# Optimization experiments

Hardware: AMD Instinct MI355X
Metric: run time of the kernel (lower is better)

Reference implementation:

```python
import jax, jax.numpy as jnp
import numpy as np
from jax import lax

BLANK = 0
LOGZERO = -1e30  # finite stand-in for -inf (keeps grads NaN-free, exact in fp32 logaddexp)


def setup_inputs() -> dict:
    key = jax.random.key(0)
    k1, k2 = jax.random.split(key)
    T, B, V, S = 512, 32, 4096, 128
    logits = jax.random.normal(k1, (T, B, V), dtype=jnp.float32)
    log_probs = jax.nn.log_softmax(logits, axis=-1)
    targets = jax.random.randint(k2, (B, S), 1, V, dtype=jnp.int32)  # avoid blank label
    input_lengths = jnp.full((B,), T, dtype=jnp.int32)   # must be >= 2*S+1
    target_lengths = jnp.full((B,), S, dtype=jnp.int32)
    return {"log_probs": log_probs, "targets": targets,
            "input_lengths": input_lengths, "target_lengths": target_lengths}


def _shift_right(a, n):
    # a: (B, L) log-space; shift states right by n, filling with log(0)
    pad = jnp.full(a.shape[:-1] + (n,), LOGZERO, dtype=a.dtype)
    return jnp.concatenate([pad, a[..., :-n]], axis=-1)


def _ctc_log_likelihood(log_probs, targets, input_lengths, target_lengths):
    # Vectorized CTC forward (alpha) recursion over the blank-interleaved trellis.
    # Mathematically identical to the per-sample bounded DP in the torch module:
    # states outside the reachability bounds carry log(0) / never feed the terminal sum.
    T, B, V = log_probs.shape
    S = targets.shape[1]
    L = 2 * S + 1
    blanked = jnp.full((B, L), BLANK, dtype=jnp.int32).at[:, 1::2].set(targets)
    # emission log-prob of each trellis state at each time: (T, B, L)
    emit = jnp.take_along_axis(log_probs, jnp.broadcast_to(blanked[None], (T, B, L)), axis=2)
    idx = jnp.arange(L)
    # skip transition (j-2 -> j) allowed for label states whose label differs from previous label
    skip = (idx % 2 == 1) & (idx >= 2) & (blanked != jnp.roll(blanked, 2, axis=1))  # (B, L)

    alpha0 = jnp.full((B, L), LOGZERO, dtype=log_probs.dtype)
    alpha0 = alpha0.at[:, 0].set(emit[0, :, 0]).at[:, 1].set(emit[0, :, 1])

    def step(alpha, xs):
        emit_t, t = xs  # emit_t: (B, L)
        pre = jnp.logaddexp(alpha, _shift_right(alpha, 1))
        pre = jnp.where(skip, jnp.logaddexp(pre, _shift_right(alpha, 2)), pre)
        new = emit_t + pre
        new = jnp.where((t < input_lengths)[:, None], new, alpha)  # freeze past each sample's length
        return new, None

    alpha, _ = lax.scan(step, alpha0, (emit[1:], jnp.arange(1, T)))
    b = jnp.arange(B)
    end = 2 * target_lengths  # final blank state index per sample
    ll = jnp.logaddexp(alpha[b, end], alpha[b, end - 1])  # log p(target | input)
    return ll


def reference(log_probs, targets, input_lengths, target_lengths):
    ll = _ctc_log_likelihood(log_probs, targets, input_lengths, target_lengths)
    B = log_probs.shape[1]
    # faithful to the module's 'mean' branch: (ret / target_lengths / B).sum()  (NOT negated)
    return (ll / target_lengths.astype(ll.dtype) / B).sum()
```

## Files before the change

kernel.cpp:

```cpp
#include <hip/hip_runtime.h>
#include <hip/hip_bf16.h>
#include <cstdint>

typedef unsigned short u16;
typedef uint32_t u32;

constexpr int Tc = 512, Bc = 32, Vc = 4096, Sc = 128;
constexpr int BOOST = 13;
constexpr int DPF = 16;
constexpr float LOG2E = 1.4426950408889634f;
constexpr float LN2 = 0.6931471805599453f;

__device__ __forceinline__ float bfs(u32 s) { return __uint_as_float(s << 16); }
__device__ __forceinline__ float bflo(u32 p) { return __uint_as_float(p << 16); }
__device__ __forceinline__ float bfhi(u32 p) { return __uint_as_float(p & 0xffff0000u); }

__device__ __forceinline__ u16 f2bf(float f) {
    __hip_bfloat16 h = __float2bfloat16(f);
    return *reinterpret_cast<u16*>(&h);
}

__global__ __launch_bounds__(128) void k_gather(const float* __restrict__ lp,
                                                const int* __restrict__ tgt,
                                                u16* __restrict__ emitT,
                                                u16* __restrict__ blankT) {
    const int t = blockIdx.x;
    const int b = blockIdx.y;
    const float* row = lp + ((size_t)t * Bc + b) * Vc;
    const int s = threadIdx.x;
    const int lab = tgt[b * Sc + s];
    const float e = __builtin_amdgcn_exp2f(fmaf(row[lab], LOG2E, (float)BOOST));
    emitT[((size_t)b * Tc + t) * Sc + s] = f2bf(e);
    if (s == 0) {
        const float eb = __builtin_amdgcn_exp2f(fmaf(row[0], LOG2E, (float)BOOST));
        blankT[(size_t)b * Tc + t] = f2bf(eb);
    }
}

template <int CTRL, int RMASK>
__device__ __forceinline__ float dppmax(float v) {
    int t = __builtin_amdgcn_update_dpp(__float_as_int(v), __float_as_int(v),
                                        CTRL, RMASK, 0xf, false);
    return fmaxf(v, __int_as_float(t));
}
__device__ __forceinline__ float wave_max_bcast(float v) {
    v = dppmax<0x111, 0xf>(v);
    v = dppmax<0x112, 0xf>(v);
    v = dppmax<0x114, 0xf>(v);
    v = dppmax<0x118, 0xf>(v);
    v = dppmax<0x142, 0xa>(v);
    v = dppmax<0x143, 0xc>(v);
    return __int_as_float(__builtin_amdgcn_readlane(__float_as_int(v), 63));
}

__global__ __launch_bounds__(64) void k_ctc(const u16* __restrict__ emitT,
                                            const u16* __restrict__ blankT,
                                            const int* __restrict__ tgt,
                                            const int* __restrict__ in_len,
                                            const int* __restrict__ tg_len,
                                            float* __restrict__ out) {
    const int b = blockIdx.x;
    const int lane = threadIdx.x;
    const u32* prow = reinterpret_cast<const u32*>(emitT + (size_t)b * Tc * Sc);
    const u16* brow = blankT + (size_t)b * Tc;

    const int tg0 = tgt[b * Sc + 2 * lane];
    const int tg1 = tgt[b * Sc + 2 * lane + 1];
    const int tgm = (lane > 0) ? tgt[b * Sc + 2 * lane - 1] : tg0;
    const float m1 = (lane > 0 && tg0 != tgm) ? 1.f : 0.f;
    const float m3 = (tg1 != tg0) ? 1.f : 0.f;
    const float sel = (lane == 63) ? 1.f : 0.f;

    const int steps = min(in_len[b], Tc) - 1;

    const u32 p0 = prow[lane];
    float a0 = (lane == 0) ? bfs(brow[0]) : 0.f;
    float a1 = (lane == 0) ? bflo(p0) : 0.f;
    float a2 = 0.f, a3 = 0.f, a4 = 0.f;
    int e_acc = 0;

    u32 pk[DPF];
    u32 bk[DPF];
#pragma unroll
    for (int d = 0; d < DPF; ++d) {
        int tt = 1 + d;
        if (tt > steps) tt = (steps > 0) ? steps : 0;
        pk[d] = prow[(size_t)tt * 64 + lane];
        bk[d] = brow[tt];
    }

#define STEP(d) {                                                   \
        const float e1 = bflo(pk[d]);                               \
        const float e3 = bfhi(pk[d]);                               \
        const float ebl = bfs(bk[d]);                               \
        int tn = t + DPF; if (tn > steps) tn = steps;               \
        pk[d] = prow[(size_t)tn * 64 + lane];                       \
        bk[d] = brow[tn];                                           \
        float sh = __shfl_up(a3, 1);                                \
        if (lane == 0) sh = 0.f;                                    \
        const float s01 = a0 + a1;                                  \
        const float s12 = a1 + a2;                                  \
        const float s23 = a2 + a3;                                  \
        const float n0 = ebl * (a0 + sh);                           \
        const float n1 = e1 * fmaf(m1, sh, s01);                    \
        const float n2 = ebl * s12;                                 \
        const float n3 = e3 * fmaf(m3, a1, s23);                    \
        const float n4 = ebl * fmaf(sel, a3, a4);                   \
        const bool live = (t <= steps);                             \
        a0 = live ? n0 : a0; a1 = live ? n1 : a1;                   \
        a2 = live ? n2 : a2; a3 = live ? n3 : a3;                   \
        a4 = live ? n4 : a4;                                        \
        ++t; }

#define RENORM() {                                                  \
        float m = fmaxf(fmaxf(fmaxf(a0, a1), fmaxf(a2, a3)), a4);   \
        m = wave_max_bcast(m);                                      \
        int e = (int)((__float_as_uint(m) >> 23) & 0xffu) - 127;    \
        float scale = __uint_as_float((u32)(127 - e) << 23);        \
        a0 *= scale; a1 *= scale; a2 *= scale;                      \
        a3 *= scale; a4 *= scale;                                   \
        e_acc += e; }

    int t = 1;
    const int ngroups = (steps + 7) / 8;
    const int npair = (ngroups + 1) / 2;
    for (int gp = 0; gp < npair; ++gp) {
#pragma unroll
        for (int d = 0; d < 8; ++d) STEP(d)
        RENORM()
#pragma unroll
        for (int d = 8; d < 16; ++d) STEP(d)
        RENORM()
    }
#undef STEP
#undef RENORM

    __shared__ float sa[257];
    sa[4 * lane + 0] = a0;
    sa[4 * lane + 1] = a1;
    sa[4 * lane + 2] = a2;
    sa[4 * lane + 3] = a3;
    if (lane == 63) sa[256] = a4;
    __syncthreads();
    if (lane == 0) {
        const int tl = tg_len[b];
        const int ei = 2 * tl;
        const float ssum = sa[ei] + sa[ei - 1];
        const float ll = __logf(ssum) +
                         LN2 * ((float)e_acc - (float)BOOST * (float)(steps + 1));
        atomicAdd(out, ll / (float)tl / (float)Bc);
    }
}

extern "C" void kernel_launch(void* const* d_in, const int* in_sizes, int n_in,
                              void* d_out, int out_size, void* d_ws, size_t ws_size,
                              hipStream_t stream) {
    const float* lp = (const float*)d_in[0];
    const int* tgt = (const int*)d_in[1];
    const int* in_len = (const int*)d_in[2];
    const int* tg_len = (const int*)d_in[3];

    char* ws = (char*)d_ws;
    u16* blankT = (u16*)ws;
    u16* emitT = (u16*)(ws + 64 * 1024);

    (void)hipMemsetAsync(d_out, 0, sizeof(float), stream);
    k_gather<<<dim3(Tc, Bc), 128, 0, stream>>>(lp, tgt, emitT, blankT);
    k_ctc<<<Bc, 64, 0, stream>>>(emitT, blankT, tgt, in_len, tg_len, (float*)d_out);
}
```

Measured before the change: 384.2 us.

## Stage log-prob rows in LDS, keep blank emissions in fp32, streamline the CTC step loop

The gather kernel now copies each full vocabulary row into shared memory with coalesced float4 loads, then gathers label emissions from LDS. Before, each thread gathered directly from global memory at random label offsets. Blank emissions are stored and read as fp32 instead of bf16. In the recurrence, the lane shift moves from __shfl_up to a DPP row-shift that fills lane 0 with zero. The steady-state loop drops the per-step liveness selects and index clamps, with a separate guarded tail block handling the last 16 steps. The trade-off: the gather reads the whole 256 MB tensor densely, and the unclamped prefetch reads one time step past the last valid one.

```diff
diff --git a/kernel.cpp b/kernel.cpp
--- a/kernel.cpp
+++ b/kernel.cpp
@@ -11,7 +11,6 @@
 constexpr float LOG2E = 1.4426950408889634f;
 constexpr float LN2 = 0.6931471805599453f;
 
-__device__ __forceinline__ float bfs(u32 s) { return __uint_as_float(s << 16); }
 __device__ __forceinline__ float bflo(u32 p) { return __uint_as_float(p << 16); }
 __device__ __forceinline__ float bfhi(u32 p) { return __uint_as_float(p & 0xffff0000u); }
 
@@ -20,20 +19,28 @@
     return *reinterpret_cast<u16*>(&h);
 }
 
-__global__ __launch_bounds__(128) void k_gather(const float* __restrict__ lp,
+__global__ __launch_bounds__(256) void k_gather(const float* __restrict__ lp,
                                                 const int* __restrict__ tgt,
                                                 u16* __restrict__ emitT,
-                                                u16* __restrict__ blankT) {
+                                                float* __restrict__ blankT) {
+    __shared__ float row[Vc];
     const int t = blockIdx.x;
     const int b = blockIdx.y;
-    const float* row = lp + ((size_t)t * Bc + b) * Vc;
+    const float4* src4 = reinterpret_cast<const float4*>(lp + ((size_t)t * Bc + b) * Vc);
+    float4* row4 = reinterpret_cast<float4*>(row);
+#pragma unroll
+    for (int i = 0; i < Vc / 4 / 256; ++i)
+        row4[threadIdx.x + i * 256] = src4[threadIdx.x + i * 256];
+    __syncthreads();
     const int s = threadIdx.x;
-    const int lab = tgt[b * Sc + s];
-    const float e = __builtin_amdgcn_exp2f(fmaf(row[lab], LOG2E, (float)BOOST));
-    emitT[((size_t)b * Tc + t) * Sc + s] = f2bf(e);
+    if (s < Sc) {
+        const int lab = tgt[b * Sc + s];
+        const float e = __builtin_amdgcn_exp2f(fmaf(row[lab], LOG2E, (float)BOOST));
+        emitT[((size_t)b * Tc + t) * Sc + s] = f2bf(e);
+    }
     if (s == 0) {
-        const float eb = __builtin_amdgcn_exp2f(fmaf(row[0], LOG2E, (float)BOOST));
-        blankT[(size_t)b * Tc + t] = f2bf(eb);
+        blankT[(size_t)b * Tc + t] =
+            __builtin_amdgcn_exp2f(fmaf(row[0], LOG2E, (float)BOOST));
     }
 }
 
@@ -53,8 +60,13 @@
     return __int_as_float(__builtin_amdgcn_readlane(__float_as_int(v), 63));
 }
 
+__device__ __forceinline__ float wave_shr1(float v) {
+    return __int_as_float(__builtin_amdgcn_update_dpp(
+        0, __float_as_int(v), 0x138, 0xf, 0xf, true));
+}
+
 __global__ __launch_bounds__(64) void k_ctc(const u16* __restrict__ emitT,
-                                            const u16* __restrict__ blankT,
+                                            const float* __restrict__ blankT,
                                             const int* __restrict__ tgt,
                                             const int* __restrict__ in_len,
                                             const int* __restrict__ tg_len,
@@ -62,7 +74,7 @@
     const int b = blockIdx.x;
     const int lane = threadIdx.x;
     const u32* prow = reinterpret_cast<const u32*>(emitT + (size_t)b * Tc * Sc);
-    const u16* brow = blankT + (size_t)b * Tc;
+    const float* brow = blankT + (size_t)b * Tc;
 
     const int tg0 = tgt[b * Sc + 2 * lane];
     const int tg1 = tgt[b * Sc + 2 * lane + 1];
@@ -74,30 +86,41 @@
     const int steps = min(in_len[b], Tc) - 1;
 
     const u32 p0 = prow[lane];
-    float a0 = (lane == 0) ? bfs(brow[0]) : 0.f;
+    float a0 = (lane == 0) ? brow[0] : 0.f;
     float a1 = (lane == 0) ? bflo(p0) : 0.f;
     float a2 = 0.f, a3 = 0.f, a4 = 0.f;
     int e_acc = 0;
 
     u32 pk[DPF];
-    u32 bk[DPF];
+    float bk[DPF];
 #pragma unroll
     for (int d = 0; d < DPF; ++d) {
-        int tt = 1 + d;
-        if (tt > steps) tt = (steps > 0) ? steps : 0;
-        pk[d] = prow[(size_t)tt * 64 + lane];
-        bk[d] = brow[tt];
+        pk[d] = prow[(size_t)(1 + d) * 64 + lane];
+        bk[d] = brow[1 + d];
     }
 
-#define STEP(d) {                                                   \
+#define STEP_N(d) {                                                 \
         const float e1 = bflo(pk[d]);                               \
         const float e3 = bfhi(pk[d]);                               \
-        const float ebl = bfs(bk[d]);                               \
-        int tn = t + DPF; if (tn > steps) tn = steps;               \
-        pk[d] = prow[(size_t)tn * 64 + lane];                       \
-        bk[d] = brow[tn];                                           \
-        float sh = __shfl_up(a3, 1);                                \
-        if (lane == 0) sh = 0.f;                                    \
+        const float ebl = bk[d];                                    \
+        pk[d] = prow[(size_t)(t + DPF) * 64 + lane];                \
+        bk[d] = brow[t + DPF];                                      \
+        const float sh = wave_shr1(a3);                             \
+        const float s01 = a0 + a1;                                  \
+        const float s12 = a1 + a2;                                  \
+        const float s23 = a2 + a3;                                  \
+        const float n0 = ebl * (a0 + sh);                           \
+        const float n1 = e1 * fmaf(m1, sh, s01);                    \
+        const float n3 = e3 * fmaf(m3, a1, s23);                    \
+        a4 = ebl * fmaf(sel, a3, a4);                               \
+        a0 = n0; a1 = n1; a2 = ebl * s12; a3 = n3;                  \
+        ++t; }
+
+#define STEP_T(d) {                                                 \
+        const float e1 = bflo(pk[d]);                               \
+        const float e3 = bfhi(pk[d]);                               \
+        const float ebl = bk[d];                                    \
+        const float sh = wave_shr1(a3);                             \
         const float s01 = a0 + a1;                                  \
         const float s12 = a1 + a2;                                  \
         const float s23 = a2 + a3;                                  \
@@ -122,17 +145,23 @@
         e_acc += e; }
 
     int t = 1;
-    const int ngroups = (steps + 7) / 8;
-    const int npair = (ngroups + 1) / 2;
-    for (int gp = 0; gp < npair; ++gp) {
+    const int nfull = steps >> 4;
+    for (int g = 0; g < nfull; ++g) {
 #pragma unroll
-        for (int d = 0; d < 8; ++d) STEP(d)
+        for (int d = 0; d < 8; ++d) STEP_N(d)
         RENORM()
 #pragma unroll
-        for (int d = 8; d < 16; ++d) STEP(d)
+        for (int d = 8; d < 16; ++d) STEP_N(d)
         RENORM()
     }
-#undef STEP
+#pragma unroll
+    for (int d = 0; d < 8; ++d) STEP_T(d)
+    RENORM()
+#pragma unroll
+    for (int d = 8; d < 16; ++d) STEP_T(d)
+    RENORM()
+#undef STEP_N
+#undef STEP_T
 #undef RENORM
 
     __shared__ float sa[257];
@@ -161,10 +190,10 @@
     const int* tg_len = (const int*)d_in[3];
 
     char* ws = (char*)d_ws;
-    u16* blankT = (u16*)ws;
-    u16* emitT = (u16*)(ws + 64 * 1024);
+    float* blankT = (float*)ws;
+    u16* emitT = (u16*)(ws + 128 * 1024);
 
     (void)hipMemsetAsync(d_out, 0, sizeof(float), stream);
-    k_gather<<<dim3(Tc, Bc), 128, 0, stream>>>(lp, tgt, emitT, blankT);
+    k_gather<<<dim3(Tc, Bc), 256, 0, stream>>>(lp, tgt, emitT, blankT);
     k_ctc<<<Bc, 64, 0, stream>>>(emitT, blankT, tgt, in_len, tg_len, (float*)d_out);
 }
```

Result: no change. 379.7 us (-1.2%).

## Coalesce emission gather via cache-line staging and streamline CTC recursion loop

Applied to the files above, without the earlier changes.

The gather kernel now finds the distinct 64-byte lines touched by each sample's labels, loads them with coalesced float4 reads into shared memory, and picks the emissions from there. This replaces scattered per-label reads. The recursion kernel now keeps the blank emissions in fp32, fetches them per 64 steps and broadcasts them with readlane. It uses a DPP row shift instead of shfl_up, a 32-deep register prefetch ring, and drops the liveness selects on full 64-step blocks. This adds bookkeeping, shared memory and barriers to the gather kernel and makes the prefetch read past the trellis end in workspace.

```diff
diff --git a/kernel.cpp b/kernel.cpp
--- a/kernel.cpp
+++ b/kernel.cpp
@@ -7,33 +7,77 @@
 
 constexpr int Tc = 512, Bc = 32, Vc = 4096, Sc = 128;
 constexpr int BOOST = 13;
-constexpr int DPF = 16;
+constexpr int BSTRIDE = 576;
 constexpr float LOG2E = 1.4426950408889634f;
 constexpr float LN2 = 0.6931471805599453f;
 
-__device__ __forceinline__ float bfs(u32 s) { return __uint_as_float(s << 16); }
 __device__ __forceinline__ float bflo(u32 p) { return __uint_as_float(p << 16); }
 __device__ __forceinline__ float bfhi(u32 p) { return __uint_as_float(p & 0xffff0000u); }
 
-__device__ __forceinline__ u16 f2bf(float f) {
+__device__ __forceinline__ u32 f2bf_bits(float f) {
     __hip_bfloat16 h = __float2bfloat16(f);
-    return *reinterpret_cast<u16*>(&h);
-}
-
-__global__ __launch_bounds__(128) void k_gather(const float* __restrict__ lp,
+    return (u32)(*reinterpret_cast<u16*>(&h));
+}
+
+#define RLF(v, i) __int_as_float(__builtin_amdgcn_readlane(__float_as_int(v), (i)))
+
+__global__ __launch_bounds__(256) void k_gather(const float* __restrict__ lp,
                                                 const int* __restrict__ tgt,
-                                                u16* __restrict__ emitT,
-                                                u16* __restrict__ blankT) {
+                                                u32* __restrict__ emitT,
+                                                float* __restrict__ blankT) {
+    __shared__ u32 bm[8];
+    __shared__ u16 wbase[8];
+    __shared__ int sn;
+    __shared__ u16 rank[256];
+    __shared__ u16 slines[136];
+    __shared__ u16 lpos[Sc];
+    __shared__ __align__(16) float vals[130 * 16];
+
     const int t = blockIdx.x;
     const int b = blockIdx.y;
+    const int tid = threadIdx.x;
+
+    if (tid < 8) bm[tid] = (tid == 0) ? 1u : 0u;
+    __syncthreads();
+    int lab = 0;
+    if (tid < Sc) {
+        lab = tgt[b * Sc + tid];
+        const int ln = lab >> 4;
+        atomicOr(&bm[ln >> 5], 1u << (ln & 31));
+    }
+    __syncthreads();
+    if (tid == 0) {
+        int acc = 0;
+        for (int w = 0; w < 8; ++w) { wbase[w] = (u16)acc; acc += __popc(bm[w]); }
+        sn = acc;
+    }
+    __syncthreads();
+    {
+        const u32 w = bm[tid >> 5];
+        if (w & (1u << (tid & 31))) {
+            const int r = wbase[tid >> 5] + __popc(w & ((1u << (tid & 31)) - 1u));
+            slines[r] = (u16)tid;
+            rank[tid] = (u16)r;
+        }
+    }
+    __syncthreads();
+    if (tid < Sc) lpos[tid] = (u16)(rank[lab >> 4] * 16 + (lab & 15));
+    const int n = sn;
     const float* row = lp + ((size_t)t * Bc + b) * Vc;
-    const int s = threadIdx.x;
-    const int lab = tgt[b * Sc + s];
-    const float e = __builtin_amdgcn_exp2f(fmaf(row[lab], LOG2E, (float)BOOST));
-    emitT[((size_t)b * Tc + t) * Sc + s] = f2bf(e);
-    if (s == 0) {
-        const float eb = __builtin_amdgcn_exp2f(fmaf(row[0], LOG2E, (float)BOOST));
-        blankT[(size_t)b * Tc + t] = f2bf(eb);
+    for (int c = tid; c < n * 4; c += 256) {
+        const int line = (int)slines[c >> 2];
+        *reinterpret_cast<float4*>(&vals[c * 4]) =
+            *reinterpret_cast<const float4*>(row + line * 16 + (c & 3) * 4);
+    }
+    __syncthreads();
+    u32* orow = emitT + ((size_t)b * Tc + t) * 64;
+    if (tid < 64) {
+        const float e0 = __builtin_amdgcn_exp2f(fmaf(vals[lpos[2 * tid]], LOG2E, (float)BOOST));
+        const float e1 = __builtin_amdgcn_exp2f(fmaf(vals[lpos[2 * tid + 1]], LOG2E, (float)BOOST));
+        orow[tid] = f2bf_bits(e0) | (f2bf_bits(e1) << 16);
+    } else if (tid == 64) {
+        blankT[b * BSTRIDE + t] =
+            __builtin_amdgcn_exp2f(fmaf(vals[0], LOG2E, (float)BOOST));
     }
 }
 
@@ -53,16 +97,21 @@
     return __int_as_float(__builtin_amdgcn_readlane(__float_as_int(v), 63));
 }
 
-__global__ __launch_bounds__(64) void k_ctc(const u16* __restrict__ emitT,
-                                            const u16* __restrict__ blankT,
+__device__ __forceinline__ float wave_shr1(float v) {
+    return __int_as_float(__builtin_amdgcn_update_dpp(
+        0, __float_as_int(v), 0x138, 0xf, 0xf, true));
+}
+
+__global__ __launch_bounds__(64) void k_ctc(const u32* __restrict__ emitT,
+                                            const float* __restrict__ blankT,
                                             const int* __restrict__ tgt,
                                             const int* __restrict__ in_len,
                                             const int* __restrict__ tg_len,
                                             float* __restrict__ out) {
     const int b = blockIdx.x;
     const int lane = threadIdx.x;
-    const u32* prow = reinterpret_cast<const u32*>(emitT + (size_t)b * Tc * Sc);
-    const u16* brow = blankT + (size_t)b * Tc;
+    const u32* p = emitT + (size_t)b * Tc * 64;
+    const float* brow = blankT + b * BSTRIDE;
 
     const int tg0 = tgt[b * Sc + 2 * lane];
     const int tg1 = tgt[b * Sc + 2 * lane + 1];
@@ -73,44 +122,19 @@
 
     const int steps = min(in_len[b], Tc) - 1;
 
-    const u32 p0 = prow[lane];
-    float a0 = (lane == 0) ? bfs(brow[0]) : 0.f;
+    const u32 p0 = p[lane];
+    float a0 = (lane == 0) ? brow[0] : 0.f;
     float a1 = (lane == 0) ? bflo(p0) : 0.f;
     float a2 = 0.f, a3 = 0.f, a4 = 0.f;
     int e_acc = 0;
 
-    u32 pk[DPF];
-    u32 bk[DPF];
+    u32 pk[32];
+    const u32* pr = p + 64;
 #pragma unroll
-    for (int d = 0; d < DPF; ++d) {
-        int tt = 1 + d;
-        if (tt > steps) tt = (steps > 0) ? steps : 0;
-        pk[d] = prow[(size_t)tt * 64 + lane];
-        bk[d] = brow[tt];
-    }
-
-#define STEP(d) {                                                   \
-        const float e1 = bflo(pk[d]);                               \
-        const float e3 = bfhi(pk[d]);                               \
-        const float ebl = bfs(bk[d]);                               \
-        int tn = t + DPF; if (tn > steps) tn = steps;               \
-        pk[d] = prow[(size_t)tn * 64 + lane];                       \
-        bk[d] = brow[tn];                                           \
-        float sh = __shfl_up(a3, 1);                                \
-        if (lane == 0) sh = 0.f;                                    \
-        const float s01 = a0 + a1;                                  \
-        const float s12 = a1 + a2;                                  \
-        const float s23 = a2 + a3;                                  \
-        const float n0 = ebl * (a0 + sh);                           \
-        const float n1 = e1 * fmaf(m1, sh, s01);                    \
-        const float n2 = ebl * s12;                                 \
-        const float n3 = e3 * fmaf(m3, a1, s23);                    \
-        const float n4 = ebl * fmaf(sel, a3, a4);                   \
-        const bool live = (t <= steps);                             \
-        a0 = live ? n0 : a0; a1 = live ? n1 : a1;                   \
-        a2 = live ? n2 : a2; a3 = live ? n3 : a3;                   \
-        a4 = live ? n4 : a4;                                        \
-        ++t; }
+    for (int d = 0; d < 32; ++d) pk[d] = pr[d * 64 + lane];
+    const u32* pg = p + (size_t)33 * 64;
+
+    float blkc = brow[1 + lane];
 
 #define RENORM() {                                                  \
         float m = fmaxf(fmaxf(fmaxf(a0, a1), fmaxf(a2, a3)), a4);   \
@@ -121,18 +145,67 @@
         a3 *= scale; a4 *= scale;                                   \
         e_acc += e; }
 
-    int t = 1;
-    const int ngroups = (steps + 7) / 8;
-    const int npair = (ngroups + 1) / 2;
-    for (int gp = 0; gp < npair; ++gp) {
-#pragma unroll
-        for (int d = 0; d < 8; ++d) STEP(d)
-        RENORM()
-#pragma unroll
-        for (int d = 8; d < 16; ++d) STEP(d)
-        RENORM()
-    }
-#undef STEP
+#define GROUP_N(g) {                                                \
+        const int H = ((g) & 1) * 16;                               \
+        const int BI = (g) * 16;                                    \
+        _Pragma("unroll")                                           \
+        for (int d = 0; d < 16; ++d) {                              \
+            const u32 pv = pk[H + d];                               \
+            pk[H + d] = pg[d * 64 + lane];                          \
+            const float ebl = RLF(blkc, BI + d);                    \
+            const float e1 = bflo(pv);                              \
+            const float e3 = bfhi(pv);                              \
+            const float sh = wave_shr1(a3);                         \
+            const float s01 = a0 + a1;                              \
+            const float s12 = a1 + a2;                              \
+            const float s23 = a2 + a3;                              \
+            const float n0 = ebl * (a0 + sh);                       \
+            const float n1 = e1 * fmaf(m1, sh, s01);                \
+            const float n3 = e3 * fmaf(m3, a1, s23);                \
+            a4 = ebl * fmaf(sel, a3, a4);                           \
+            a0 = n0; a1 = n1; a2 = ebl * s12; a3 = n3;              \
+            if (d == 7 || d == 15) RENORM()                         \
+        }                                                           \
+        pg += 16 * 64; }
+
+#define GROUP_T(g) {                                                \
+        const int H = ((g) & 1) * 16;                               \
+        const int BI = (g) * 16;                                    \
+        _Pragma("unroll")                                           \
+        for (int d = 0; d < 16; ++d) {                              \
+            const u32 pv = pk[H + d];                               \
+            pk[H + d] = pg[d * 64 + lane];                          \
+            const float ebl = RLF(blkc, BI + d);                    \
+            const float e1 = bflo(pv);                              \
+            const float e3 = bfhi(pv);                              \
+            const float sh = wave_shr1(a3);                         \
+            const float s01 = a0 + a1;                              \
+            const float s12 = a1 + a2;                              \
+            const float s23 = a2 + a3;                              \
+            const float n0 = ebl * (a0 + sh);                       \
+            const float n1 = e1 * fmaf(m1, sh, s01);                \
+            const float n2 = ebl * s12;                             \
+            const float n3 = e3 * fmaf(m3, a1, s23);                \
+            const float n4 = ebl * fmaf(sel, a3, a4);               \
+            const bool live = (t <= steps);                         \
+            a0 = live ? n0 : a0; a1 = live ? n1 : a1;               \
+            a2 = live ? n2 : a2; a3 = live ? n3 : a3;               \
+            a4 = live ? n4 : a4;                                    \
+            ++t;                                                    \
+            if (d == 7 || d == 15) RENORM()                         \
+        }                                                           \
+        pg += 16 * 64; }
+
+    const int nsb = steps >> 6;
+    for (int sb = 0; sb < nsb; ++sb) {
+        const float blkn = brow[(sb + 1) * 64 + 1 + lane];
+        GROUP_N(0) GROUP_N(1) GROUP_N(2) GROUP_N(3)
+        blkc = blkn;
+    }
+    int t = (nsb << 6) + 1;
+    GROUP_T(0) GROUP_T(1) GROUP_T(2) GROUP_T(3)
+#undef GROUP_N
+#undef GROUP_T
 #undef RENORM
 
     __shared__ float sa[257];
@@ -161,10 +234,10 @@
     const int* tg_len = (const int*)d_in[3];
 
     char* ws = (char*)d_ws;
-    u16* blankT = (u16*)ws;
-    u16* emitT = (u16*)(ws + 64 * 1024);
+    float* blankT = (float*)ws;
+    u32* emitT = (u32*)(ws + 128 * 1024);
 
     (void)hipMemsetAsync(d_out, 0, sizeof(float), stream);
-    k_gather<<<dim3(Tc, Bc), 128, 0, stream>>>(lp, tgt, emitT, blankT);
+    k_gather<<<dim3(Tc, Bc), 256, 0, stream>>>(lp, tgt, emitT, blankT);
     k_ctc<<<Bc, 64, 0, stream>>>(emitT, blankT, tgt, in_len, tg_len, (float*)d_out);
 }
```

After: 364.2 us. 1.05x faster.
